# Kernel optimization log

Hardware: AMD Instinct MI355X
Metric: run time of the kernel (lower is better)

The kernel has to match this reference:

```python
import jax, jax.numpy as jnp
import numpy as np

N = 100000        # nodes
E = 1600000       # edges (avg degree 16)
D = 128           # feature dim (in_dim == out_dim)
L = 3             # num_layers
P = 8             # num_parts


def setup_inputs() -> dict:
    key = jax.random.key(0)
    k1, k2, k3, k4, k5, k6 = jax.random.split(key, 6)
    edge_row = jnp.sort(jax.random.randint(k1, (E,), 0, N))
    edge_col = jax.random.randint(k2, (E,), 0, N)
    edge_vals = jax.random.uniform(k3, (E,), dtype=jnp.float32)
    x = jax.random.normal(k4, (N, D), dtype=jnp.float32)
    stacked_params = jax.random.normal(k5, (L, D, D, P), dtype=jnp.float32)
    layer_weights = jax.random.normal(k6, (L, P), dtype=jnp.float32)
    return {"edge_row": edge_row, "edge_col": edge_col, "edge_vals": edge_vals,
            "x": x, "stacked_params": stacked_params, "layer_weights": layer_weights}


def reference(edge_row, edge_col, edge_vals, x, stacked_params, layer_weights):
    n = x.shape[0]
    num_layers = stacked_params.shape[0]
    h = x
    for i in range(num_layers):
        # sparse adj.spmm(h): gather source features, scale by edge value, sum per row
        msg = h[edge_col] * edge_vals[:, None]                       # [E, D]
        ax = jax.ops.segment_sum(msg, edge_row, num_segments=n)      # [N, D]
        # MyLinear: softmax over the num_parts weight, contract parts dim
        w = jax.nn.softmax(layer_weights[i])                         # [P]
        ww = jnp.einsum('oip,p->oi', stacked_params[i], w)           # [D_out, D_in]
        h = ax @ ww.T                                                # [N, D_out]
        if i < num_layers - 1:
            h = jax.nn.relu(h)
    return h
```

## Files before the change

### kernel.cpp

```cpp
#include <hip/hip_runtime.h>
#include <cstdint>

#define D 128
#define P 8
#define L 3

typedef __attribute__((ext_vector_type(8))) _Float16 f16x8;
typedef __attribute__((ext_vector_type(4))) float    f32x4;

__global__ void build_row_ptr(const int* __restrict__ er, int* __restrict__ rp, int n, int e) {
    int r = blockIdx.x * blockDim.x + threadIdx.x;
    if (r > n) return;
    int lo = 0, hi = e;
    while (lo < hi) {
        int mid = (lo + hi) >> 1;
        if (er[mid] < r) lo = mid + 1; else hi = mid;
    }
    rp[r] = lo;
}

__global__ void build_ww(const float* __restrict__ sp, const float* __restrict__ lw,
                         _Float16* __restrict__ wwB) {
    int idx = blockIdx.x * blockDim.x + threadIdx.x;
    if (idx >= L * D * D) return;
    int l = idx / (D * D);
    int rem = idx - l * D * D;
    int o = rem / D;
    int i = rem - o * D;
    float wv[P];
    float m = -1e30f;
#pragma unroll
    for (int p = 0; p < P; p++) { wv[p] = lw[l * P + p]; m = fmaxf(m, wv[p]); }
    float s = 0.f;
#pragma unroll
    for (int p = 0; p < P; p++) { wv[p] = __expf(wv[p] - m); s += wv[p]; }
    float inv = 1.0f / s;
    const float* spp = sp + ((size_t)(l * D + o) * D + i) * P;
    float acc = 0.f;
#pragma unroll
    for (int p = 0; p < P; p++) acc += spp[p] * wv[p];
    int kt = i >> 5, kp = i & 31;
    wwB[(((l * 4 + kt) * D + o) << 5) + kp] = (_Float16)(acc * inv);
}

static __device__ __forceinline__ void mfma_store16(const _Float16 (*s_h)[136],
                                                    const _Float16* __restrict__ wwB_l,
                                                    _Float16* __restrict__ y,
                                                    int row0, int n, int tid) {
    const int w = tid >> 6, lane = tid & 63;
    const int quad = lane >> 4, l16 = lane & 15;
    f32x4 acc[2] = {};
#pragma unroll
    for (int kt = 0; kt < 4; kt++) {
        f16x8 af = *(const f16x8*)&s_h[l16][kt * 32 + quad * 8];
#pragma unroll
        for (int c = 0; c < 2; c++) {
            const int ct = w * 2 + c;
            f16x8 bf = *(const f16x8*)&wwB_l[((kt * D + ct * 16 + l16) << 5) + quad * 8];
            acc[c] = __builtin_amdgcn_mfma_f32_16x16x32_f16(af, bf, acc[c], 0, 0, 0);
        }
    }
#pragma unroll
    for (int c = 0; c < 2; c++) {
        const int ct = w * 2 + c;
#pragma unroll
        for (int rg = 0; rg < 4; rg++) {
            int row = row0 + quad * 4 + rg;
            if (row < n) y[row * D + ct * 16 + l16] = (_Float16)acc[c][rg];
        }
    }
}

__global__ __launch_bounds__(256, 8)
void gemm_x32(const float* __restrict__ x, const _Float16* __restrict__ wwB_l,
              _Float16* __restrict__ y, int n) {
    __shared__ _Float16 s_h[16][136];
    const int tid = threadIdx.x;
    const int row0 = blockIdx.x * 16;
    const int c8 = (tid & 15) * 8;
    {
        int r = tid >> 4;
        int row = row0 + r;
        float4 v0 = {}, v1 = {};
        if (row < n) {
            v0 = *(const float4*)&x[row * D + c8];
            v1 = *(const float4*)&x[row * D + c8 + 4];
        }
        f16x8 h;
        h[0] = (_Float16)v0.x; h[1] = (_Float16)v0.y;
        h[2] = (_Float16)v0.z; h[3] = (_Float16)v0.w;
        h[4] = (_Float16)v1.x; h[5] = (_Float16)v1.y;
        h[6] = (_Float16)v1.z; h[7] = (_Float16)v1.w;
        *(f16x8*)&s_h[r][c8] = h;
    }
    __syncthreads();
    mfma_store16(s_h, wwB_l, y, row0, n, tid);
}

static __device__ __forceinline__ void gather_row(float (&a)[8],
                                                  const _Float16* __restrict__ y,
                                                  const int* __restrict__ col,
                                                  const float* __restrict__ vals,
                                                  int e, int e1, int c8) {
    union U8 { uint4 u; _Float16 h[8]; };
    for (; e + 8 <= e1; e += 8) {
        int c[8]; float v[8]; U8 g[8];
#pragma unroll
        for (int j = 0; j < 8; j++) { c[j] = col[e + j]; v[j] = vals[e + j]; }
#pragma unroll
        for (int j = 0; j < 8; j++) g[j].u = *(const uint4*)&y[c[j] * D + c8];
#pragma unroll
        for (int j = 0; j < 8; j++)
#pragma unroll
            for (int k = 0; k < 8; k++) a[k] += v[j] * (float)g[j].h[k];
    }
    for (; e + 4 <= e1; e += 4) {
        int c[4]; float v[4]; U8 g[4];
#pragma unroll
        for (int j = 0; j < 4; j++) { c[j] = col[e + j]; v[j] = vals[e + j]; }
#pragma unroll
        for (int j = 0; j < 4; j++) g[j].u = *(const uint4*)&y[c[j] * D + c8];
#pragma unroll
        for (int j = 0; j < 4; j++)
#pragma unroll
            for (int k = 0; k < 8; k++) a[k] += v[j] * (float)g[j].h[k];
    }
    for (; e < e1; e++) {
        U8 g; g.u = *(const uint4*)&y[col[e] * D + c8];
        float v = vals[e];
#pragma unroll
        for (int k = 0; k < 8; k++) a[k] += v * (float)g.h[k];
    }
}

__global__ __launch_bounds__(256, 8)
void fused_layer(const _Float16* __restrict__ yprev, const int* __restrict__ rp,
                 const int* __restrict__ col, const float* __restrict__ vals,
                 const _Float16* __restrict__ wwB_l, _Float16* __restrict__ ynext, int n) {
    __shared__ _Float16 s_h[16][136];
    const int tid = threadIdx.x;
    const int row0 = blockIdx.x * 16;
    const int sg = tid >> 4;
    const int c8 = (tid & 15) * 8;
    {
        int r = row0 + sg;
        float a[8] = {0.f, 0.f, 0.f, 0.f, 0.f, 0.f, 0.f, 0.f};
        if (r < n) gather_row(a, yprev, col, vals, rp[r], rp[r + 1], c8);
        f16x8 o;
#pragma unroll
        for (int k = 0; k < 8; k++) o[k] = (_Float16)fmaxf(a[k], 0.f);
        *(f16x8*)&s_h[sg][c8] = o;
    }
    __syncthreads();
    mfma_store16(s_h, wwB_l, ynext, row0, n, tid);
}

__global__ __launch_bounds__(256, 8)
void spmm_f32(const _Float16* __restrict__ y, const int* __restrict__ rp,
              const int* __restrict__ col, const float* __restrict__ vals,
              float* __restrict__ out, int n) {
    const int tid = threadIdx.x;
    const int r = blockIdx.x * 16 + (tid >> 4);
    const int c8 = (tid & 15) * 8;
    if (r >= n) return;
    float a[8] = {0.f, 0.f, 0.f, 0.f, 0.f, 0.f, 0.f, 0.f};
    gather_row(a, y, col, vals, rp[r], rp[r + 1], c8);
    *(float4*)&out[r * D + c8]     = make_float4(a[0], a[1], a[2], a[3]);
    *(float4*)&out[r * D + c8 + 4] = make_float4(a[4], a[5], a[6], a[7]);
}

extern "C" void kernel_launch(void* const* d_in, const int* in_sizes, int n_in,
                              void* d_out, int out_size, void* d_ws, size_t ws_size,
                              hipStream_t stream) {
    const int*   edge_row  = (const int*)d_in[0];
    const int*   edge_col  = (const int*)d_in[1];
    const float* edge_vals = (const float*)d_in[2];
    const float* x         = (const float*)d_in[3];
    const float* sp        = (const float*)d_in[4];
    const float* lw        = (const float*)d_in[5];
    float* out = (float*)d_out;

    const int E_ = in_sizes[0];
    const int N_ = in_sizes[3] / D;

    char* ws = (char*)d_ws;
    int* row_ptr = (int*)ws;
    size_t off = (((size_t)(N_ + 1) * sizeof(int)) + 255) & ~(size_t)255;
    _Float16* wwB = (_Float16*)(ws + off);
    off += (size_t)L * 4 * D * 32 * sizeof(_Float16);
    off = (off + 255) & ~(size_t)255;
    _Float16* bufA = (_Float16*)(ws + off);
    off += (size_t)N_ * D * sizeof(_Float16);
    _Float16* bufB = (_Float16*)(ws + off);

    build_row_ptr<<<(N_ + 1 + 255) / 256, 256, 0, stream>>>(edge_row, row_ptr, N_, E_);
    build_ww<<<(L * D * D + 255) / 256, 256, 0, stream>>>(sp, lw, wwB);

    const int sblk = (N_ + 15) / 16;
    const int WWL = 4 * D * 32;

    gemm_x32<<<sblk, 256, 0, stream>>>(x, wwB, bufA, N_);
    fused_layer<<<sblk, 256, 0, stream>>>(bufA, row_ptr, edge_col, edge_vals,
                                          wwB + WWL,     bufB, N_);
    fused_layer<<<sblk, 256, 0, stream>>>(bufB, row_ptr, edge_col, edge_vals,
                                          wwB + 2 * WWL, bufA, N_);
    spmm_f32<<<sblk, 256, 0, stream>>>(bufA, row_ptr, edge_col, edge_vals, out, N_);
}
```

Measured before the change: 316.7 us.

## Pack edge col and fp16 value into one word; gather rows per wavefront

```diff
diff --git a/kernel.cpp b/kernel.cpp
--- a/kernel.cpp
+++ b/kernel.cpp
@@ -8,15 +8,26 @@
 typedef __attribute__((ext_vector_type(8))) _Float16 f16x8;
 typedef __attribute__((ext_vector_type(4))) float    f32x4;
 
-__global__ void build_row_ptr(const int* __restrict__ er, int* __restrict__ rp, int n, int e) {
-    int r = blockIdx.x * blockDim.x + threadIdx.x;
-    if (r > n) return;
-    int lo = 0, hi = e;
-    while (lo < hi) {
-        int mid = (lo + hi) >> 1;
-        if (er[mid] < r) lo = mid + 1; else hi = mid;
-    }
-    rp[r] = lo;
+__global__ void prep_edges(const int* __restrict__ er, const int* __restrict__ col,
+                           const float* __restrict__ vals,
+                           int* __restrict__ rp, uint32_t* __restrict__ epk,
+                           int n, int e) {
+    int i = blockIdx.x * blockDim.x + threadIdx.x;
+    if (i >= e) return;
+    union { _Float16 h; uint16_t u; } v;
+    v.h = (_Float16)vals[i];
+    epk[i] = ((uint32_t)col[i] << 15) | (uint32_t)(v.u & 0x7FFFu);
+
+    int cur = er[i];
+    if (i == 0) {
+        for (int r = 0; r <= cur; r++) rp[r] = 0;
+    } else {
+        int prev = er[i - 1];
+        for (int r = prev + 1; r <= cur; r++) rp[r] = i;
+    }
+    if (i == e - 1) {
+        for (int r = cur + 1; r <= n; r++) rp[r] = e;
+    }
 }
 
 __global__ void build_ww(const float* __restrict__ sp, const float* __restrict__ lw,
@@ -97,59 +108,64 @@
     mfma_store16(s_h, wwB_l, y, row0, n, tid);
 }
 
-static __device__ __forceinline__ void gather_row(float (&a)[8],
-                                                  const _Float16* __restrict__ y,
-                                                  const int* __restrict__ col,
-                                                  const float* __restrict__ vals,
-                                                  int e, int e1, int c8) {
-    union U8 { uint4 u; _Float16 h[8]; };
-    for (; e + 8 <= e1; e += 8) {
-        int c[8]; float v[8]; U8 g[8];
-#pragma unroll
-        for (int j = 0; j < 8; j++) { c[j] = col[e + j]; v[j] = vals[e + j]; }
-#pragma unroll
-        for (int j = 0; j < 8; j++) g[j].u = *(const uint4*)&y[c[j] * D + c8];
-#pragma unroll
-        for (int j = 0; j < 8; j++)
-#pragma unroll
-            for (int k = 0; k < 8; k++) a[k] += v[j] * (float)g[j].h[k];
-    }
-    for (; e + 4 <= e1; e += 4) {
-        int c[4]; float v[4]; U8 g[4];
-#pragma unroll
-        for (int j = 0; j < 4; j++) { c[j] = col[e + j]; v[j] = vals[e + j]; }
-#pragma unroll
-        for (int j = 0; j < 4; j++) g[j].u = *(const uint4*)&y[c[j] * D + c8];
-#pragma unroll
-        for (int j = 0; j < 4; j++)
-#pragma unroll
-            for (int k = 0; k < 8; k++) a[k] += v[j] * (float)g[j].h[k];
-    }
-    for (; e < e1; e++) {
-        U8 g; g.u = *(const uint4*)&y[col[e] * D + c8];
-        float v = vals[e];
-#pragma unroll
-        for (int k = 0; k < 8; k++) a[k] += v * (float)g.h[k];
-    }
+template<int NB>
+static __device__ __forceinline__ void gather_chunk(float& a0, float& a1,
+                                                    const _Float16* __restrict__ y,
+                                                    const uint32_t* __restrict__ epk,
+                                                    int e, int l2) {
+    uint32_t m[NB];
+#pragma unroll
+    for (int j = 0; j < NB; j++) m[j] = epk[e + j];
+    uint32_t g[NB];
+#pragma unroll
+    for (int j = 0; j < NB; j++) {
+        uint32_t off = (m[j] >> 15) * (uint32_t)D + (uint32_t)l2;
+        g[j] = *(const uint32_t*)&y[off];
+    }
+#pragma unroll
+    for (int j = 0; j < NB; j++) {
+        union { uint32_t u; _Float16 h[2]; } gg; gg.u = g[j];
+        union { uint16_t u; _Float16 h; } vv; vv.u = (uint16_t)(m[j] & 0x7FFFu);
+        float vf = (float)vv.h;
+        a0 += vf * (float)gg.h[0];
+        a1 += vf * (float)gg.h[1];
+    }
+}
+
+static __device__ __forceinline__ void gather_row64(float& a0, float& a1,
+                                                    const _Float16* __restrict__ y,
+                                                    const uint32_t* __restrict__ epk,
+                                                    int e, int e1, int l2) {
+    for (; e + 16 <= e1; e += 16) gather_chunk<16>(a0, a1, y, epk, e, l2);
+    if (e + 8 <= e1) { gather_chunk<8>(a0, a1, y, epk, e, l2); e += 8; }
+    if (e + 4 <= e1) { gather_chunk<4>(a0, a1, y, epk, e, l2); e += 4; }
+    for (; e < e1; e++) gather_chunk<1>(a0, a1, y, epk, e, l2);
 }
 
 __global__ __launch_bounds__(256, 8)
 void fused_layer(const _Float16* __restrict__ yprev, const int* __restrict__ rp,
-                 const int* __restrict__ col, const float* __restrict__ vals,
-                 const _Float16* __restrict__ wwB_l, _Float16* __restrict__ ynext, int n) {
+                 const uint32_t* __restrict__ epk, const _Float16* __restrict__ wwB_l,
+                 _Float16* __restrict__ ynext, int n) {
     __shared__ _Float16 s_h[16][136];
     const int tid = threadIdx.x;
+    const int lane = tid & 63;
+    const int l2 = lane * 2;
+    const int w = __builtin_amdgcn_readfirstlane(tid >> 6);
     const int row0 = blockIdx.x * 16;
-    const int sg = tid >> 4;
-    const int c8 = (tid & 15) * 8;
-    {
-        int r = row0 + sg;
-        float a[8] = {0.f, 0.f, 0.f, 0.f, 0.f, 0.f, 0.f, 0.f};
-        if (r < n) gather_row(a, yprev, col, vals, rp[r], rp[r + 1], c8);
-        f16x8 o;
-#pragma unroll
-        for (int k = 0; k < 8; k++) o[k] = (_Float16)fmaxf(a[k], 0.f);
-        *(f16x8*)&s_h[sg][c8] = o;
+    const int rbase = row0 + w * 4;
+#pragma unroll 1
+    for (int q = 0; q < 4; q++) {
+        const int r = rbase + q;
+        float a0 = 0.f, a1 = 0.f;
+        if (r < n) {
+            int e  = __builtin_amdgcn_readfirstlane(rp[r]);
+            int e1 = __builtin_amdgcn_readfirstlane(rp[r + 1]);
+            gather_row64(a0, a1, yprev, epk, e, e1, l2);
+        }
+        union { uint32_t u; _Float16 h[2]; } o;
+        o.h[0] = (_Float16)fmaxf(a0, 0.f);
+        o.h[1] = (_Float16)fmaxf(a1, 0.f);
+        *(uint32_t*)&s_h[w * 4 + q][l2] = o.u;
     }
     __syncthreads();
     mfma_store16(s_h, wwB_l, ynext, row0, n, tid);
@@ -157,16 +173,22 @@
 
 __global__ __launch_bounds__(256, 8)
 void spmm_f32(const _Float16* __restrict__ y, const int* __restrict__ rp,
-              const int* __restrict__ col, const float* __restrict__ vals,
-              float* __restrict__ out, int n) {
+              const uint32_t* __restrict__ epk, float* __restrict__ out, int n) {
     const int tid = threadIdx.x;
-    const int r = blockIdx.x * 16 + (tid >> 4);
-    const int c8 = (tid & 15) * 8;
-    if (r >= n) return;
-    float a[8] = {0.f, 0.f, 0.f, 0.f, 0.f, 0.f, 0.f, 0.f};
-    gather_row(a, y, col, vals, rp[r], rp[r + 1], c8);
-    *(float4*)&out[r * D + c8]     = make_float4(a[0], a[1], a[2], a[3]);
-    *(float4*)&out[r * D + c8 + 4] = make_float4(a[4], a[5], a[6], a[7]);
+    const int lane = tid & 63;
+    const int l2 = lane * 2;
+    const int w = __builtin_amdgcn_readfirstlane(tid >> 6);
+    const int rbase = blockIdx.x * 16 + w * 4;
+#pragma unroll 1
+    for (int q = 0; q < 4; q++) {
+        const int r = rbase + q;
+        if (r >= n) continue;
+        float a0 = 0.f, a1 = 0.f;
+        int e  = __builtin_amdgcn_readfirstlane(rp[r]);
+        int e1 = __builtin_amdgcn_readfirstlane(rp[r + 1]);
+        gather_row64(a0, a1, y, epk, e, e1, l2);
+        *(float2*)&out[(size_t)r * D + l2] = make_float2(a0, a1);
+    }
 }
 
 extern "C" void kernel_launch(void* const* d_in, const int* in_sizes, int n_in,
@@ -186,6 +208,9 @@
     char* ws = (char*)d_ws;
     int* row_ptr = (int*)ws;
     size_t off = (((size_t)(N_ + 1) * sizeof(int)) + 255) & ~(size_t)255;
+    uint32_t* epk = (uint32_t*)(ws + off);
+    off += (size_t)E_ * sizeof(uint32_t);
+    off = (off + 255) & ~(size_t)255;
     _Float16* wwB = (_Float16*)(ws + off);
     off += (size_t)L * 4 * D * 32 * sizeof(_Float16);
     off = (off + 255) & ~(size_t)255;
@@ -193,16 +218,15 @@
     off += (size_t)N_ * D * sizeof(_Float16);
     _Float16* bufB = (_Float16*)(ws + off);
 
-    build_row_ptr<<<(N_ + 1 + 255) / 256, 256, 0, stream>>>(edge_row, row_ptr, N_, E_);
+    prep_edges<<<(E_ + 255) / 256, 256, 0, stream>>>(edge_row, edge_col, edge_vals,
+                                                     row_ptr, epk, N_, E_);
     build_ww<<<(L * D * D + 255) / 256, 256, 0, stream>>>(sp, lw, wwB);
 
     const int sblk = (N_ + 15) / 16;
     const int WWL = 4 * D * 32;
 
     gemm_x32<<<sblk, 256, 0, stream>>>(x, wwB, bufA, N_);
-    fused_layer<<<sblk, 256, 0, stream>>>(bufA, row_ptr, edge_col, edge_vals,
-                                          wwB + WWL,     bufB, N_);
-    fused_layer<<<sblk, 256, 0, stream>>>(bufB, row_ptr, edge_col, edge_vals,
-                                          wwB + 2 * WWL, bufA, N_);
-    spmm_f32<<<sblk, 256, 0, stream>>>(bufA, row_ptr, edge_col, edge_vals, out, N_);
-}
+    fused_layer<<<sblk, 256, 0, stream>>>(bufA, row_ptr, epk, wwB + WWL,     bufB, N_);
+    fused_layer<<<sblk, 256, 0, stream>>>(bufB, row_ptr, epk, wwB + 2 * WWL, bufA, N_);
+    spmm_f32<<<sblk, 256, 0, stream>>>(bufA, row_ptr, epk, out, N_);
+}
```

After: 317.6 us. Within noise of the previous version (+0.3%).
